# Performance work log

Hardware: AMD Instinct MI355X
Metric: run time of the kernel (lower is better)

The kernel has to match this reference:

```python
import jax, jax.numpy as jnp
import numpy as np

TEMPERATURE = 8.0


def setup_inputs() -> dict:
    key = jax.random.key(0)
    kq, kk, kv, kc = jax.random.split(key, 4)
    B, L, D = 4, 4096, 64
    q = jax.random.normal(kq, (B, L, D), dtype=jnp.float32)
    k = jax.random.normal(kk, (B, L, D), dtype=jnp.float32)
    v = jax.random.normal(kv, (B, L, D), dtype=jnp.float32)
    # vectors = stack(softmax(randn(d_v)), softmax(randn(d_v)))  (dim=0 softmax over d_v)
    raw = jax.random.normal(kc, (2, D), dtype=jnp.float32)
    vectors = jax.nn.softmax(raw, axis=1)
    return {"q": q, "k": k, "v": v, "vectors": vectors}


def reference(q, k, v, vectors):
    # Original builds diagonal core tensors cores[t,t,t] = vectors[.,t] for t < min(dimen, len_q),
    # then einsum('pqk,bip,bjq,bkr->bijr') and sums over j. With a diagonal core this collapses to:
    #   out[b,i,r] = sum_{t<m} q[b,i,t] * w[t] * ksum[b,t] * v[b,t,r]
    # where w = 0.5*(c1+c2)/temperature and ksum[b,t] = sum_j k[b,j,t].
    B, L, D = q.shape
    m = min(D, L)  # static python int
    w = 0.5 * (vectors[0, :m] + vectors[1, :m]) / TEMPERATURE          # [m]
    ksum = jnp.sum(k[:, :, :m], axis=1)                                 # [B, m]
    coef = w[None, :] * ksum                                            # [B, m]
    output = jnp.einsum('bit,bt,btr->bir', q[:, :, :m], coef, v[:, :m, :])  # [B, L, D]
    attn = jnp.einsum('bid,bjd->bij', q, k)                             # [B, L, L]
    return (output, attn)
```

## Files before the change

### kernel.cpp

```cpp
#include <hip/hip_runtime.h>
#include <stdint.h>

#define BB 4
#define LL 4096
#define DD 64

typedef __attribute__((ext_vector_type(8))) short bf16x8;
typedef __attribute__((ext_vector_type(4))) float f32x4;

static __device__ __forceinline__ unsigned short f2bf(float x) {
    unsigned int u = __builtin_bit_cast(unsigned int, x);
    u += 0x7fffu + ((u >> 16) & 1u);
    return (unsigned short)(u >> 16);
}

__global__ __launch_bounds__(256) void convert_kernel(
    const float* __restrict__ q, const float* __restrict__ k,
    unsigned short* __restrict__ qbf, unsigned short* __restrict__ kbf,
    float* __restrict__ part)
{
    const int NBQ = (BB * LL * DD) / 2048;
    int bid = blockIdx.x;
    bool is_k = bid >= NBQ;
    const float* src = is_k ? k : q;
    unsigned short* dst = is_k ? kbf : qbf;
    int cb = is_k ? (bid - NBQ) : bid;
    int tid = threadIdx.x;

    size_t idx0 = (size_t)cb * 2048 + (size_t)tid * 8;
    float4 f0 = *(const float4*)(src + idx0);
    float4 f1 = *(const float4*)(src + idx0 + 4);
    float f[8] = {f0.x, f0.y, f0.z, f0.w, f1.x, f1.y, f1.z, f1.w};

    unsigned short u[8];
    #pragma unroll
    for (int e = 0; e < 8; e++) u[e] = f2bf(f[e]);
    uint4 pk;
    pk.x = (unsigned)u[0] | ((unsigned)u[1] << 16);
    pk.y = (unsigned)u[2] | ((unsigned)u[3] << 16);
    pk.z = (unsigned)u[4] | ((unsigned)u[5] << 16);
    pk.w = (unsigned)u[6] | ((unsigned)u[7] << 16);
    *(uint4*)(dst + idx0) = pk;

    if (is_k) {
        __shared__ float red[256][8];
        #pragma unroll
        for (int e = 0; e < 8; e++) red[tid][e] = f[e];
        __syncthreads();
        if (tid < 64) {
            int g = tid >> 3, e = tid & 7;
            float s = 0.f;
            #pragma unroll
            for (int r = 0; r < 32; r++) s += red[r * 8 + g][e];
            part[(size_t)cb * 64 + tid] = s;
        }
    }
}

__global__ __launch_bounds__(256) void out_kernel(
    const float* __restrict__ q, const float* __restrict__ v,
    const float* __restrict__ vec, const float* __restrict__ part,
    float* __restrict__ out)
{
    __shared__ float csh[64];
    __shared__ float Vl[64][65];
    __shared__ float qs[32][65];

    int bid = blockIdx.x;
    int b   = bid >> 7;
    int i0  = (bid & 127) << 5;
    int tid = threadIdx.x;

    if (tid < 64) {
        const float* pp = part + (size_t)b * 128 * 64 + tid;
        float s = 0.f;
        #pragma unroll 8
        for (int c = 0; c < 128; c++) s += pp[c * 64];
        csh[tid] = 0.0625f * (vec[tid] + vec[64 + tid]) * s;
    }
    {
        const float* vb = v + (size_t)b * LL * DD;
        #pragma unroll
        for (int it = 0; it < 4; it++) {
            int idx4 = it * 256 + tid;
            int t  = idx4 >> 4;
            int r4 = (idx4 & 15) << 2;
            float4 w = *(const float4*)(vb + (size_t)idx4 * 4);
            Vl[t][r4 + 0] = w.x; Vl[t][r4 + 1] = w.y;
            Vl[t][r4 + 2] = w.z; Vl[t][r4 + 3] = w.w;
        }
    }
    __syncthreads();
    {
        const float* qb = q + (size_t)b * LL * DD;
        int row = tid >> 3;
        int t0  = (tid & 7) << 3;
        const float* src = qb + (size_t)(i0 + row) * DD + t0;
        float4 a0 = *(const float4*)(src);
        float4 a1 = *(const float4*)(src + 4);
        float fa[8] = {a0.x,a0.y,a0.z,a0.w,a1.x,a1.y,a1.z,a1.w};
        #pragma unroll
        for (int e = 0; e < 8; e++) qs[row][t0 + e] = fa[e] * csh[t0 + e];
    }
    __syncthreads();

    int ii = tid >> 3;
    int g  = tid & 7;
    float acc[8] = {0,0,0,0,0,0,0,0};
    #pragma unroll 8
    for (int t = 0; t < 64; t++) {
        float qv = qs[ii][t];
        #pragma unroll
        for (int j = 0; j < 8; j++) acc[j] += qv * Vl[t][g * 8 + j];
    }
    float* op = out + (size_t)b * LL * DD + (size_t)(i0 + ii) * DD + g * 8;
    float4 s0 = {acc[0], acc[1], acc[2], acc[3]};
    float4 s1 = {acc[4], acc[5], acc[6], acc[7]};
    *(float4*)(op)     = s0;
    *(float4*)(op + 4) = s1;
}

__global__ __launch_bounds__(256) void attn_kernel(
    const unsigned short* __restrict__ qbf,
    const unsigned short* __restrict__ kbf,
    float* __restrict__ attn)
{
    int bid = blockIdx.x;
    int swz = (bid & 7) * 512 + (bid >> 3);
    int b   = swz >> 10;
    int rem = swz & 1023;
    int ti  = rem >> 5;
    int tj  = rem & 31;

    int tid  = threadIdx.x;
    int wid  = tid >> 6;
    int lane = tid & 63;
    int wm = wid >> 1, wn = wid & 1;
    int row0 = ti * 128 + wm * 64;
    int col0 = tj * 128 + wn * 64;

    const unsigned short* qb = qbf + (size_t)b * LL * DD;
    const unsigned short* kb = kbf + (size_t)b * LL * DD;

    int lr = lane & 15;
    int lk = (lane >> 4) * 8;

    f32x4 acc[4][4];
    #pragma unroll
    for (int m = 0; m < 4; m++)
        #pragma unroll
        for (int n = 0; n < 4; n++)
            acc[m][n] = (f32x4){0.f, 0.f, 0.f, 0.f};

    #pragma unroll
    for (int kk = 0; kk < 2; kk++) {
        int k0 = kk * 32 + lk;
        bf16x8 a[4], bf[4];
        #pragma unroll
        for (int m = 0; m < 4; m++)
            a[m] = *(const bf16x8*)(qb + (size_t)(row0 + m * 16 + lr) * DD + k0);
        #pragma unroll
        for (int n = 0; n < 4; n++)
            bf[n] = *(const bf16x8*)(kb + (size_t)(col0 + n * 16 + lr) * DD + k0);
        #pragma unroll
        for (int m = 0; m < 4; m++)
            #pragma unroll
            for (int n = 0; n < 4; n++)
                acc[m][n] = __builtin_amdgcn_mfma_f32_16x16x32_bf16(
                    a[m], bf[n], acc[m][n], 0, 0, 0);
    }

    float* ab = attn + (size_t)b * LL * LL;
    int rbase = (lane >> 4) * 4;
    #pragma unroll
    for (int m = 0; m < 4; m++) {
        #pragma unroll
        for (int reg = 0; reg < 4; reg++) {
            size_t roff = (size_t)(row0 + m * 16 + rbase + reg) * LL + col0 + lr;
            #pragma unroll
            for (int n = 0; n < 4; n++)
                ab[roff + n * 16] = acc[m][n][reg];
        }
    }
}

extern "C" void kernel_launch(void* const* d_in, const int* in_sizes, int n_in,
                              void* d_out, int out_size, void* d_ws, size_t ws_size,
                              hipStream_t stream) {
    const float* q   = (const float*)d_in[0];
    const float* k   = (const float*)d_in[1];
    const float* v   = (const float*)d_in[2];
    const float* vec = (const float*)d_in[3];

    float* out  = (float*)d_out;
    float* attn = out + (size_t)BB * LL * DD;

    unsigned short* qbf = (unsigned short*)d_ws;
    unsigned short* kbf = qbf + (size_t)BB * LL * DD;
    float* part = (float*)(kbf + (size_t)BB * LL * DD);

    convert_kernel<<<1024, 256, 0, stream>>>(q, k, qbf, kbf, part);
    out_kernel<<<512, 256, 0, stream>>>(q, v, vec, part, out);
    attn_kernel<<<4096, 256, 0, stream>>>(qbf, kbf, attn);
}
```

Baseline: 75.32 us.

## Fuse bf16 conversion into attn kernel and store transposed tiles as vector nontemporal writes

Removes the separate q/k bf16 conversion pass and its workspace round trip by converting fp32 to bf16 inside the attention MFMA kernel, and shrinks the k column-sum pre-pass to a small reduction kernel. The MFMA operands are swapped so each lane holds four consecutive columns of a row, which allows 16-byte nontemporal stores of the 256 MB attention output instead of scalar strided stores. In exchange, every attention block re-reads fp32 inputs (twice the bytes) and repeats the conversion work redundantly across tiles.

```diff
diff --git a/kernel.cpp b/kernel.cpp
--- a/kernel.cpp
+++ b/kernel.cpp
@@ -14,46 +14,40 @@
     return (unsigned short)(u >> 16);
 }
 
-__global__ __launch_bounds__(256) void convert_kernel(
-    const float* __restrict__ q, const float* __restrict__ k,
-    unsigned short* __restrict__ qbf, unsigned short* __restrict__ kbf,
-    float* __restrict__ part)
+static __device__ __forceinline__ bf16x8 cvt8(float4 a, float4 b) {
+    bf16x8 r;
+    r[0] = (short)f2bf(a.x); r[1] = (short)f2bf(a.y);
+    r[2] = (short)f2bf(a.z); r[3] = (short)f2bf(a.w);
+    r[4] = (short)f2bf(b.x); r[5] = (short)f2bf(b.y);
+    r[6] = (short)f2bf(b.z); r[7] = (short)f2bf(b.w);
+    return r;
+}
+
+__global__ __launch_bounds__(256) void ksum_kernel(
+    const float* __restrict__ k, float* __restrict__ part)
 {
-    const int NBQ = (BB * LL * DD) / 2048;
     int bid = blockIdx.x;
-    bool is_k = bid >= NBQ;
-    const float* src = is_k ? k : q;
-    unsigned short* dst = is_k ? kbf : qbf;
-    int cb = is_k ? (bid - NBQ) : bid;
+    int b = bid >> 5, c = bid & 31;
+    const float* base = k + ((size_t)b * LL + (size_t)c * 128) * DD;
     int tid = threadIdx.x;
+    int ri = tid >> 4;
+    int c4 = (tid & 15) << 2;
 
-    size_t idx0 = (size_t)cb * 2048 + (size_t)tid * 8;
-    float4 f0 = *(const float4*)(src + idx0);
-    float4 f1 = *(const float4*)(src + idx0 + 4);
-    float f[8] = {f0.x, f0.y, f0.z, f0.w, f1.x, f1.y, f1.z, f1.w};
-
-    unsigned short u[8];
+    float4 s = {0.f, 0.f, 0.f, 0.f};
     #pragma unroll
-    for (int e = 0; e < 8; e++) u[e] = f2bf(f[e]);
-    uint4 pk;
-    pk.x = (unsigned)u[0] | ((unsigned)u[1] << 16);
-    pk.y = (unsigned)u[2] | ((unsigned)u[3] << 16);
-    pk.z = (unsigned)u[4] | ((unsigned)u[5] << 16);
-    pk.w = (unsigned)u[6] | ((unsigned)u[7] << 16);
-    *(uint4*)(dst + idx0) = pk;
-
-    if (is_k) {
-        __shared__ float red[256][8];
+    for (int it = 0; it < 8; ++it) {
+        float4 w = *(const float4*)(base + (size_t)(it * 16 + ri) * DD + c4);
+        s.x += w.x; s.y += w.y; s.z += w.z; s.w += w.w;
+    }
+    __shared__ float red[16][64];
+    red[ri][c4 + 0] = s.x; red[ri][c4 + 1] = s.y;
+    red[ri][c4 + 2] = s.z; red[ri][c4 + 3] = s.w;
+    __syncthreads();
+    if (tid < 64) {
+        float t = 0.f;
         #pragma unroll
-        for (int e = 0; e < 8; e++) red[tid][e] = f[e];
-        __syncthreads();
-        if (tid < 64) {
-            int g = tid >> 3, e = tid & 7;
-            float s = 0.f;
-            #pragma unroll
-            for (int r = 0; r < 32; r++) s += red[r * 8 + g][e];
-            part[(size_t)cb * 64 + tid] = s;
-        }
+        for (int r = 0; r < 16; ++r) t += red[r][tid];
+        part[((size_t)b * 32 + c) * 64 + tid] = t;
     }
 }
 
@@ -72,10 +66,9 @@
     int tid = threadIdx.x;
 
     if (tid < 64) {
-        const float* pp = part + (size_t)b * 128 * 64 + tid;
         float s = 0.f;
         #pragma unroll 8
-        for (int c = 0; c < 128; c++) s += pp[c * 64];
+        for (int c = 0; c < 32; ++c) s += part[((size_t)b * 32 + c) * 64 + tid];
         csh[tid] = 0.0625f * (vec[tid] + vec[64 + tid]) * s;
     }
     {
@@ -121,8 +114,8 @@
 }
 
 __global__ __launch_bounds__(256) void attn_kernel(
-    const unsigned short* __restrict__ qbf,
-    const unsigned short* __restrict__ kbf,
+    const float* __restrict__ q,
+    const float* __restrict__ k,
     float* __restrict__ attn)
 {
     int bid = blockIdx.x;
@@ -139,8 +132,8 @@
     int row0 = ti * 128 + wm * 64;
     int col0 = tj * 128 + wn * 64;
 
-    const unsigned short* qb = qbf + (size_t)b * LL * DD;
-    const unsigned short* kb = kbf + (size_t)b * LL * DD;
+    const float* qb = q + (size_t)b * LL * DD;
+    const float* kb = k + (size_t)b * LL * DD;
 
     int lr = lane & 15;
     int lk = (lane >> 4) * 8;
@@ -155,31 +148,34 @@
     #pragma unroll
     for (int kk = 0; kk < 2; kk++) {
         int k0 = kk * 32 + lk;
-        bf16x8 a[4], bf[4];
+        bf16x8 qf[4], kf[4];
         #pragma unroll
-        for (int m = 0; m < 4; m++)
-            a[m] = *(const bf16x8*)(qb + (size_t)(row0 + m * 16 + lr) * DD + k0);
+        for (int m = 0; m < 4; m++) {
+            const float* p = qb + (size_t)(row0 + m * 16 + lr) * DD + k0;
+            qf[m] = cvt8(*(const float4*)p, *(const float4*)(p + 4));
+        }
         #pragma unroll
-        for (int n = 0; n < 4; n++)
-            bf[n] = *(const bf16x8*)(kb + (size_t)(col0 + n * 16 + lr) * DD + k0);
+        for (int n = 0; n < 4; n++) {
+            const float* p = kb + (size_t)(col0 + n * 16 + lr) * DD + k0;
+            kf[n] = cvt8(*(const float4*)p, *(const float4*)(p + 4));
+        }
         #pragma unroll
         for (int m = 0; m < 4; m++)
             #pragma unroll
             for (int n = 0; n < 4; n++)
                 acc[m][n] = __builtin_amdgcn_mfma_f32_16x16x32_bf16(
-                    a[m], bf[n], acc[m][n], 0, 0, 0);
+                    kf[n], qf[m], acc[m][n], 0, 0, 0);
     }
 
     float* ab = attn + (size_t)b * LL * LL;
-    int rbase = (lane >> 4) * 4;
+    int jb = (lane >> 4) * 4;
     #pragma unroll
     for (int m = 0; m < 4; m++) {
+        size_t roff = (size_t)(row0 + m * 16 + lr) * LL;
         #pragma unroll
-        for (int reg = 0; reg < 4; reg++) {
-            size_t roff = (size_t)(row0 + m * 16 + rbase + reg) * LL + col0 + lr;
-            #pragma unroll
-            for (int n = 0; n < 4; n++)
-                ab[roff + n * 16] = acc[m][n][reg];
+        for (int n = 0; n < 4; n++) {
+            __builtin_nontemporal_store(
+                acc[m][n], (f32x4*)(ab + roff + col0 + n * 16 + jb));
         }
     }
 }
@@ -195,11 +191,9 @@
     float* out  = (float*)d_out;
     float* attn = out + (size_t)BB * LL * DD;
 
-    unsigned short* qbf = (unsigned short*)d_ws;
-    unsigned short* kbf = qbf + (size_t)BB * LL * DD;
-    float* part = (float*)(kbf + (size_t)BB * LL * DD);
+    float* part = (float*)d_ws;
 
-    convert_kernel<<<1024, 256, 0, stream>>>(q, k, qbf, kbf, part);
+    ksum_kernel<<<128, 256, 0, stream>>>(k, part);
     out_kernel<<<512, 256, 0, stream>>>(q, v, vec, part, out);
-    attn_kernel<<<4096, 256, 0, stream>>>(qbf, kbf, attn);
+    attn_kernel<<<4096, 256, 0, stream>>>(q, k, attn);
 }
```

Result: slower. 113.0 us (+50.0%).

## Restructure attn kernel into row-strip blocks with swapped MFMA operands for vector stores

Applied to the files above, without the earlier changes.

The QK^T kernel now gives each 512-thread block a 32-row strip of queries, keeps the Q fragments in registers, and loops over the key columns in chunks of 512. The MFMA operands are swapped (K as A, Q as B), so each lane's four accumulator values are contiguous in a row and can be written with one 16-byte store instead of scattered 4-byte stores. The aim is better write coalescing on the large fp32 attention output, which dominates memory traffic, and fewer redundant Q loads. The trade-off is fewer blocks (512) and less reuse of each K load across rows (32 rows instead of 128), so more K is read from cache.

```diff
diff --git a/kernel.cpp b/kernel.cpp
--- a/kernel.cpp
+++ b/kernel.cpp
@@ -120,66 +120,71 @@
     *(float4*)(op + 4) = s1;
 }
 
-__global__ __launch_bounds__(256) void attn_kernel(
+__global__ __launch_bounds__(512, 4) void attn_kernel(
     const unsigned short* __restrict__ qbf,
     const unsigned short* __restrict__ kbf,
     float* __restrict__ attn)
 {
     int bid = blockIdx.x;
-    int swz = (bid & 7) * 512 + (bid >> 3);
-    int b   = swz >> 10;
-    int rem = swz & 1023;
-    int ti  = rem >> 5;
-    int tj  = rem & 31;
+    int swz = (bid & 7) * 64 + (bid >> 3);
+    int b   = swz >> 7;
+    int ti  = swz & 127;
+    int i0  = ti * 32;
 
     int tid  = threadIdx.x;
-    int wid  = tid >> 6;
+    int w    = tid >> 6;
     int lane = tid & 63;
-    int wm = wid >> 1, wn = wid & 1;
-    int row0 = ti * 128 + wm * 64;
-    int col0 = tj * 128 + wn * 64;
+    int lr = lane & 15;
+    int g  = lane >> 4;
+    int lk = g * 8;
+    int jb = g * 4;
 
     const unsigned short* qb = qbf + (size_t)b * LL * DD;
     const unsigned short* kb = kbf + (size_t)b * LL * DD;
-
-    int lr = lane & 15;
-    int lk = (lane >> 4) * 8;
-
-    f32x4 acc[4][4];
+    float* ab = attn + (size_t)b * LL * LL;
+
+    bf16x8 qf[2][2];
     #pragma unroll
-    for (int m = 0; m < 4; m++)
+    for (int m = 0; m < 2; m++)
+        #pragma unroll
+        for (int kk = 0; kk < 2; kk++)
+            qf[m][kk] = *(const bf16x8*)(
+                qb + (size_t)(i0 + m * 16 + lr) * DD + kk * 32 + lk);
+
+    #pragma unroll
+    for (int tj = 0; tj < 8; tj++) {
+        int j0 = tj * 512 + w * 64;
+
+        bf16x8 kf[4][2];
         #pragma unroll
         for (int n = 0; n < 4; n++)
-            acc[m][n] = (f32x4){0.f, 0.f, 0.f, 0.f};
-
-    #pragma unroll
-    for (int kk = 0; kk < 2; kk++) {
-        int k0 = kk * 32 + lk;
-        bf16x8 a[4], bf[4];
-        #pragma unroll
-        for (int m = 0; m < 4; m++)
-            a[m] = *(const bf16x8*)(qb + (size_t)(row0 + m * 16 + lr) * DD + k0);
-        #pragma unroll
-        for (int n = 0; n < 4; n++)
-            bf[n] = *(const bf16x8*)(kb + (size_t)(col0 + n * 16 + lr) * DD + k0);
-        #pragma unroll
-        for (int m = 0; m < 4; m++)
+            #pragma unroll
+            for (int kk = 0; kk < 2; kk++)
+                kf[n][kk] = *(const bf16x8*)(
+                    kb + (size_t)(j0 + n * 16 + lr) * DD + kk * 32 + lk);
+
+        f32x4 acc[2][4];
+        #pragma unroll
+        for (int m = 0; m < 2; m++)
             #pragma unroll
             for (int n = 0; n < 4; n++)
-                acc[m][n] = __builtin_amdgcn_mfma_f32_16x16x32_bf16(
-                    a[m], bf[n], acc[m][n], 0, 0, 0);
-    }
-
-    float* ab = attn + (size_t)b * LL * LL;
-    int rbase = (lane >> 4) * 4;
-    #pragma unroll
-    for (int m = 0; m < 4; m++) {
-        #pragma unroll
-        for (int reg = 0; reg < 4; reg++) {
-            size_t roff = (size_t)(row0 + m * 16 + rbase + reg) * LL + col0 + lr;
+                acc[m][n] = (f32x4){0.f, 0.f, 0.f, 0.f};
+
+        #pragma unroll
+        for (int kk = 0; kk < 2; kk++)
+            #pragma unroll
+            for (int m = 0; m < 2; m++)
+                #pragma unroll
+                for (int n = 0; n < 4; n++)
+                    acc[m][n] = __builtin_amdgcn_mfma_f32_16x16x32_bf16(
+                        kf[n][kk], qf[m][kk], acc[m][n], 0, 0, 0);
+
+        #pragma unroll
+        for (int m = 0; m < 2; m++) {
+            size_t roff = (size_t)(i0 + m * 16 + lr) * LL;
             #pragma unroll
             for (int n = 0; n < 4; n++)
-                ab[roff + n * 16] = acc[m][n][reg];
+                *(f32x4*)(ab + roff + j0 + n * 16 + jb) = acc[m][n];
         }
     }
 }
@@ -201,5 +206,5 @@
 
     convert_kernel<<<1024, 256, 0, stream>>>(q, k, qbf, kbf, part);
     out_kernel<<<512, 256, 0, stream>>>(q, v, vec, part, out);
-    attn_kernel<<<4096, 256, 0, stream>>>(qbf, kbf, attn);
-}
+    attn_kernel<<<512, 512, 0, stream>>>(qbf, kbf, attn);
+}
```

Result: slower. 78.31 us (+4.0%).
